# Performance work log

Hardware: AMD Instinct MI355X
Metric: run time of the kernel (lower is better)

Reference implementation:

```python
import jax, jax.numpy as jnp
import numpy as np

B, T, S = 8, 8192, 128
VD, LD, E, H = 256, 768, 256, 8
HD = E // H
SCALE = HD ** -0.5
NEG = -9e15


def setup_inputs() -> dict:
    key = jax.random.key(0)
    ks = jax.random.split(key, 16)
    def xavier(k, shape):
        fan_in, fan_out = shape[1], shape[0]
        lim = np.sqrt(6.0 / (fan_in + fan_out))
        return jax.random.uniform(k, shape, jnp.float32, -lim, lim)
    return {
        "v": jax.random.normal(ks[0], (B, T, VD), jnp.float32),
        "l": jax.random.normal(ks[1], (B, S, LD), jnp.float32),
        "v_pos": jax.random.normal(ks[2], (B, T, VD), jnp.float32),
        "attention_mask_l": jnp.ones((B, S), jnp.int32),
        "attention_mask_v": jnp.ones((B, T), jnp.int32),
        "Wv": xavier(ks[3], (E, VD)),  "bv": jnp.zeros((E,), jnp.float32),
        "Wl": xavier(ks[4], (E, LD)),  "bl": jnp.zeros((E,), jnp.float32),
        "Wvv": xavier(ks[5], (E, VD)), "bvv": jnp.zeros((E,), jnp.float32),
        "Wvl": xavier(ks[6], (E, LD)), "bvl": jnp.zeros((E,), jnp.float32),
        "Wov": xavier(ks[7], (VD, E)), "bov": jnp.zeros((VD,), jnp.float32),
        "Wol": xavier(ks[8], (LD, E)), "bol": jnp.zeros((LD,), jnp.float32),
    }


def _heads(x):  # [B, N, E] -> [B, H, N, HD]
    Bn, N, _ = x.shape
    return x.reshape(Bn, N, H, HD).transpose(0, 2, 1, 3)


def reference(v, l, v_pos, attention_mask_l, attention_mask_v,
              Wv, bv, Wl, bl, Wvv, bvv, Wvl, bvl, Wov, bov, Wol, bol):
    # projections
    q = _heads(((v + v_pos) @ Wv.T + bv) * SCALE)   # [B,H,T,HD]
    k = _heads(l @ Wl.T + bl)                        # [B,H,S,HD]
    val_v = _heads(v @ Wvv.T + bvv)                  # [B,H,T,HD]
    val_l = _heads(l @ Wvl.T + bvl)                  # [B,H,S,HD]

    # shared score matrix
    attn = jnp.einsum("bhtd,bhsd->bhts", q, k)       # [B,H,T,S]

    # language -> vision direction (softmax over vision tokens T)
    attn_T = attn.transpose(0, 1, 3, 2)              # [B,H,S,T]
    attn_l = attn_T - jnp.max(attn_T, axis=-1, keepdims=True)
    mv = attention_mask_v.astype(jnp.float32)
    add_v = jnp.where(mv == 0, NEG, mv)[:, None, None, :]  # [B,1,1,T]
    attn_l = jax.nn.softmax(attn_l + add_v, axis=-1)

    # vision -> language direction (softmax over language tokens S)
    ml = attention_mask_l.astype(jnp.float32)
    add_l = jnp.where(ml == 0, NEG, ml)[:, None, None, :]  # [B,1,1,S]
    attn_v = jax.nn.softmax(attn + add_l, axis=-1)

    # dropout p=0.1 is identity in eval mode
    out_v = jnp.einsum("bhts,bhsd->bhtd", attn_v, val_l)  # [B,H,T,HD]
    out_l = jnp.einsum("bhst,bhtd->bhsd", attn_l, val_v)  # [B,H,S,HD]

    out_v = out_v.transpose(0, 2, 1, 3).reshape(B, T, E) @ Wov.T + bov
    out_l = out_l.transpose(0, 2, 1, 3).reshape(B, S, E) @ Wol.T + bol
    return out_v, out_l
```

## Files before the change

kernel.cpp:

```cpp
#include <hip/hip_runtime.h>

#define B_ 8
#define T_ 8192
#define S_ 128
#define VD_ 256
#define LD_ 768
#define E_ 256
#define H_ 8
#define HD_ 32
#define TC_ 8
#define SCALE_ 0.17677669529663687f
#define NEG_ -9.0e15f
#define FIXM_ 40.0f

typedef __bf16 bf16x8 __attribute__((ext_vector_type(8)));
typedef float f32x4 __attribute__((ext_vector_type(4)));
typedef unsigned int uint4v __attribute__((ext_vector_type(4)));

__device__ inline float bf2f(unsigned short u) {
    return __uint_as_float(((unsigned int)u) << 16);
}
__device__ inline unsigned short f2bf(float f) {
    unsigned int u = __float_as_uint(f);
    u = u + 0x7FFFu + ((u >> 16) & 1u);
    return (unsigned short)(u >> 16);
}
__device__ inline unsigned int pkbf(float lo, float hi) {
    unsigned short a = __builtin_bit_cast(unsigned short, (__bf16)lo);
    unsigned short b = __builtin_bit_cast(unsigned short, (__bf16)hi);
    return (unsigned int)a | ((unsigned int)b << 16);
}
__device__ inline bf16x8 lds8(const unsigned short* p) {
    uint4v v = *reinterpret_cast<const uint4v*>(p);
    return __builtin_bit_cast(bf16x8, v);
}

template<typename T>
__device__ inline uint4v load8_as_bf16(const T* p);

template<> __device__ inline uint4v load8_as_bf16<unsigned short>(const unsigned short* p) {
    return *reinterpret_cast<const uint4v*>(p);
}
template<> __device__ inline uint4v load8_as_bf16<float>(const float* p) {
    f32x4 f0 = reinterpret_cast<const f32x4*>(p)[0];
    f32x4 f1 = reinterpret_cast<const f32x4*>(p)[1];
    uint4v r;
    #pragma unroll
    for (int jj = 0; jj < 2; ++jj) {
        r[jj]     = (unsigned int)f2bf(f0[jj*2]) | ((unsigned int)f2bf(f0[jj*2+1]) << 16);
        r[jj + 2] = (unsigned int)f2bf(f1[jj*2]) | ((unsigned int)f2bf(f1[jj*2+1]) << 16);
    }
    return r;
}
__device__ inline uint4v load8_add_as_bf16(const float* p, const float* p2) {
    f32x4 a0 = reinterpret_cast<const f32x4*>(p)[0];
    f32x4 a1 = reinterpret_cast<const f32x4*>(p)[1];
    f32x4 b0 = reinterpret_cast<const f32x4*>(p2)[0];
    f32x4 b1 = reinterpret_cast<const f32x4*>(p2)[1];
    a0 += b0; a1 += b1;
    uint4v r;
    #pragma unroll
    for (int jj = 0; jj < 2; ++jj) {
        r[jj]     = (unsigned int)f2bf(a0[jj*2]) | ((unsigned int)f2bf(a0[jj*2+1]) << 16);
        r[jj + 2] = (unsigned int)f2bf(a1[jj*2]) | ((unsigned int)f2bf(a1[jj*2+1]) << 16);
    }
    return r;
}

template<typename TA, typename TW, typename TOUT, bool HAS_A2, bool SCALED>
__global__ __launch_bounds__(256) void gemm_bt(
    const TA* __restrict__ A, const TA* __restrict__ A2,
    const TW* __restrict__ W, const float* __restrict__ bias,
    TOUT* __restrict__ C, int M, int N, int K, float scale)
{
    __shared__ __align__(16) unsigned short As[64][72];
    __shared__ __align__(16) unsigned short Ws[64][72];
    const int tid  = threadIdx.x;
    const int lane = tid & 63;
    const int w    = tid >> 6;
    const int wm   = w >> 1, wn = w & 1;
    const int m0   = blockIdx.x * 64, n0 = blockIdx.y * 64;
    const int row  = tid >> 2, c0 = tid & 3;
    const int qd   = lane >> 4, lr = lane & 15;
    const f32x4 zero = {0.f, 0.f, 0.f, 0.f};
    f32x4 acc[2][2] = {{zero, zero}, {zero, zero}};

    for (int k0 = 0; k0 < K; k0 += 64) {
        #pragma unroll
        for (int cc = 0; cc < 2; ++cc) {
            int c = c0 + cc * 4;
            const TA* pa = A + (size_t)(m0 + row) * K + k0 + c * 8;
            uint4v va;
            if constexpr (HAS_A2) {
                const TA* pa2 = A2 + (size_t)(m0 + row) * K + k0 + c * 8;
                va = load8_add_as_bf16(pa, pa2);
            } else {
                va = load8_as_bf16<TA>(pa);
            }
            *reinterpret_cast<uint4v*>(&As[row][c * 8]) = va;
            const TW* pw = W + (size_t)(n0 + row) * K + k0 + c * 8;
            *reinterpret_cast<uint4v*>(&Ws[row][c * 8]) = load8_as_bf16<TW>(pw);
        }
        __syncthreads();
        #pragma unroll
        for (int ks = 0; ks < 2; ++ks) {
            bf16x8 af[2], bfr[2];
            #pragma unroll
            for (int i = 0; i < 2; ++i)
                af[i] = lds8(&As[wm * 32 + i * 16 + lr][ks * 32 + qd * 8]);
            #pragma unroll
            for (int i = 0; i < 2; ++i)
                bfr[i] = lds8(&Ws[wn * 32 + i * 16 + lr][ks * 32 + qd * 8]);
            #pragma unroll
            for (int i = 0; i < 2; ++i)
                #pragma unroll
                for (int j = 0; j < 2; ++j)
                    acc[i][j] = __builtin_amdgcn_mfma_f32_16x16x32_bf16(
                        af[i], bfr[j], acc[i][j], 0, 0, 0);
        }
        __syncthreads();
    }
    #pragma unroll
    for (int j = 0; j < 2; ++j) {
        int col = n0 + wn * 32 + j * 16 + lr;
        float bval = bias[col];
        #pragma unroll
        for (int i = 0; i < 2; ++i) {
            int r0 = m0 + wm * 32 + i * 16 + qd * 4;
            #pragma unroll
            for (int r = 0; r < 4; ++r) {
                float v = acc[i][j][r] + bval;
                if (SCALED) v *= scale;
                if constexpr (sizeof(TOUT) == 2)
                    C[(size_t)(r0 + r) * N + col] = (TOUT)f2bf(v);
                else
                    C[(size_t)(r0 + r) * N + col] = (TOUT)v;
            }
        }
    }
}

template<typename TA, typename TOUT, bool HAS_A2, bool SCALED>
__global__ __launch_bounds__(1024) void gemm_ws(
    const TA* __restrict__ A, const float* __restrict__ A2,
    const float* __restrict__ Wf, const float* __restrict__ bias,
    TOUT* __restrict__ C, float scale)
{
    __shared__ __align__(16) unsigned short Ws[256 * 256];
    const int tid  = threadIdx.x;
    const int lane = tid & 63;
    const int w    = tid >> 6;
    const int quad = lane >> 4, lr = lane & 15;

    {
        const int row = tid >> 2;
        const int g0  = tid & 3;
        #pragma unroll
        for (int i = 0; i < 8; ++i) {
            const int g  = g0 + i * 4;
            const int gs = g ^ (row & 7);
            uint4v val = load8_as_bf16<float>(Wf + (size_t)row * 256 + g * 8);
            *reinterpret_cast<uint4v*>(&Ws[row * 256 + gs * 8]) = val;
        }
    }

    const int r0   = blockIdx.x * 256 + w * 16;
    const int arow = r0 + lr;
    bf16x8 af[8];
    #pragma unroll
    for (int kq = 0; kq < 8; ++kq) {
        if constexpr (sizeof(TA) == 2) {
            af[kq] = lds8(reinterpret_cast<const unsigned short*>(A)
                          + (size_t)arow * 256 + quad * 8 + kq * 32);
        } else {
            const float* pa = reinterpret_cast<const float*>(A)
                              + (size_t)arow * 256 + quad * 8 + kq * 32;
            f32x4 a0 = reinterpret_cast<const f32x4*>(pa)[0];
            f32x4 a1 = reinterpret_cast<const f32x4*>(pa)[1];
            if constexpr (HAS_A2) {
                const float* pp = A2 + (size_t)arow * 256 + quad * 8 + kq * 32;
                a0 += reinterpret_cast<const f32x4*>(pp)[0];
                a1 += reinterpret_cast<const f32x4*>(pp)[1];
            }
            uint4v u;
            u[0] = pkbf(a0[0], a0[1]); u[1] = pkbf(a0[2], a0[3]);
            u[2] = pkbf(a1[0], a1[1]); u[3] = pkbf(a1[2], a1[3]);
            af[kq] = __builtin_bit_cast(bf16x8, u);
        }
    }
    __syncthreads();

    const f32x4 zero = {0.f, 0.f, 0.f, 0.f};
    const int swz = lr & 7;
    for (int j = 0; j < 16; ++j) {
        const unsigned short* wbase = &Ws[(j * 16 + lr) * 256];
        f32x4 acc = zero;
        #pragma unroll
        for (int kq = 0; kq < 8; ++kq) {
            const int gs = (kq * 4 + quad) ^ swz;
            bf16x8 bw = lds8(wbase + gs * 8);
            acc = __builtin_amdgcn_mfma_f32_16x16x32_bf16(af[kq], bw, acc, 0, 0, 0);
        }
        const int col = j * 16 + lr;
        const float bval = bias[col];
        #pragma unroll
        for (int r = 0; r < 4; ++r) {
            float v0 = acc[r] + bval;
            if constexpr (SCALED) v0 *= scale;
            if constexpr (sizeof(TOUT) == 2)
                C[(size_t)(r0 + quad * 4 + r) * 256 + col] = (TOUT)f2bf(v0);
            else
                C[(size_t)(r0 + quad * 4 + r) * 256 + col] = (TOUT)v0;
        }
    }
}

__global__ __launch_bounds__(256) void attn_v_kernel(
    const unsigned short* __restrict__ q, const unsigned short* __restrict__ k,
    const unsigned short* __restrict__ vall, const int* __restrict__ mask_l,
    unsigned short* __restrict__ hv)
{
    __shared__ __align__(16) unsigned short Pl[64][136];
    __shared__ __align__(16) unsigned short Vt[32][136];
    const int tid  = threadIdx.x;
    const int lane = tid & 63;
    const int w    = tid >> 6;
    const int bh   = blockIdx.y, b = bh >> 3, h = bh & 7;
    const int t0   = blockIdx.x * 64;
    const int quad = lane >> 4, lr = lane & 15;
    const f32x4 zero = {0.f, 0.f, 0.f, 0.f};

    {
        int s = tid >> 1, dh = (tid & 1) * 16;
        const unsigned short* p = vall + (size_t)(b * S_ + s) * E_ + h * HD_ + dh;
        #pragma unroll
        for (int part = 0; part < 2; ++part) {
            uint4v v = reinterpret_cast<const uint4v*>(p)[part];
            #pragma unroll
            for (int jj = 0; jj < 4; ++jj) {
                unsigned int u = v[jj];
                int d = dh + part * 8 + jj * 2;
                Vt[d][s]     = (unsigned short)(u & 0xffffu);
                Vt[d + 1][s] = (unsigned short)(u >> 16);
            }
        }
    }

    bf16x8 afq = lds8(q + (size_t)(b * T_ + t0 + w * 16 + lr) * E_ + h * HD_ + quad * 8);
    f32x4 sc[8];
    #pragma unroll
    for (int n = 0; n < 8; ++n) {
        bf16x8 bk = lds8(k + (size_t)(b * S_ + n * 16 + lr) * E_ + h * HD_ + quad * 8);
        sc[n] = __builtin_amdgcn_mfma_f32_16x16x32_bf16(afq, bk, zero, 0, 0, 0);
    }
    #pragma unroll
    for (int n = 0; n < 8; ++n) {
        int s = n * 16 + lr;
        int mv = mask_l[b * S_ + s];
        float ad = (mv == 0) ? NEG_ : (float)mv;
        #pragma unroll
        for (int r = 0; r < 4; ++r) sc[n][r] += ad;
    }
    #pragma unroll
    for (int r = 0; r < 4; ++r) {
        float sum = 0.f;
        #pragma unroll
        for (int n = 0; n < 8; ++n) { float e = __expf(sc[n][r] - FIXM_); sc[n][r] = e; sum += e; }
        for (int off = 1; off < 16; off <<= 1) sum += __shfl_xor(sum, off);
        float inv = 1.0f / sum;
        #pragma unroll
        for (int n = 0; n < 8; ++n) sc[n][r] *= inv;
    }
    #pragma unroll
    for (int n = 0; n < 8; ++n)
        #pragma unroll
        for (int r = 0; r < 4; ++r)
            Pl[w * 16 + quad * 4 + r][n * 16 + lr] = f2bf(sc[n][r]);
    __syncthreads();
    f32x4 av[2] = {zero, zero};
    #pragma unroll
    for (int ks = 0; ks < 4; ++ks) {
        bf16x8 ap = lds8(&Pl[w * 16 + lr][ks * 32 + quad * 8]);
        #pragma unroll
        for (int nn = 0; nn < 2; ++nn) {
            bf16x8 bv = lds8(&Vt[nn * 16 + lr][ks * 32 + quad * 8]);
            av[nn] = __builtin_amdgcn_mfma_f32_16x16x32_bf16(ap, bv, av[nn], 0, 0, 0);
        }
    }
    #pragma unroll
    for (int nn = 0; nn < 2; ++nn)
        #pragma unroll
        for (int r = 0; r < 4; ++r) {
            int t = t0 + w * 16 + quad * 4 + r;
            hv[(size_t)(b * T_ + t) * E_ + h * HD_ + nn * 16 + lr] = f2bf(av[nn][r]);
        }
}

__global__ __launch_bounds__(512) void attn_l_kernel(
    const unsigned short* __restrict__ q, const unsigned short* __restrict__ k,
    const unsigned short* __restrict__ valv, const int* __restrict__ mask_v,
    float* __restrict__ pM, float* __restrict__ pL, float* __restrict__ pA)
{
    __shared__ __align__(16) unsigned short Et[128][136];
    __shared__ __align__(16) unsigned short Vt[32][136];
    const int tid  = threadIdx.x;
    const int lane = tid & 63;
    const int w    = tid >> 6;
    const int bh   = blockIdx.y, b = bh >> 3, h = bh & 7;
    const int chunk = blockIdx.x;
    const int quad = lane >> 4, lr = lane & 15;
    const int sw0  = w * 16;
    const f32x4 zero = {0.f, 0.f, 0.f, 0.f};

    bf16x8 kf = lds8(k + (size_t)(b * S_ + sw0 + lr) * E_ + h * HD_ + quad * 8);

    float lrun[4] = {0.f, 0.f, 0.f, 0.f};
    f32x4 accl[2] = {zero, zero};

    const int titer = T_ / TC_ / 128;
    for (int it = 0; it < titer; ++it) {
        int t0 = chunk * (T_ / TC_) + it * 128;
        __syncthreads();
        {
            int t = tid >> 2, dq = tid & 3;
            const unsigned short* p = valv + (size_t)(b * T_ + t0 + t) * E_ + h * HD_ + dq * 8;
            uint4v v = *reinterpret_cast<const uint4v*>(p);
            #pragma unroll
            for (int jj = 0; jj < 4; ++jj) {
                unsigned int u = v[jj];
                Vt[dq * 8 + jj * 2][t]     = (unsigned short)(u & 0xffffu);
                Vt[dq * 8 + jj * 2 + 1][t] = (unsigned short)(u >> 16);
            }
        }
        f32x4 sc[8];
        #pragma unroll
        for (int n = 0; n < 8; ++n) {
            bf16x8 qf = lds8(q + (size_t)(b * T_ + t0 + n * 16 + lr) * E_ + h * HD_ + quad * 8);
            sc[n] = __builtin_amdgcn_mfma_f32_16x16x32_bf16(kf, qf, zero, 0, 0, 0);
        }
        #pragma unroll
        for (int n = 0; n < 8; ++n) {
            int t = t0 + n * 16 + lr;
            int mv = mask_v[b * T_ + t];
            float ad = (mv == 0) ? NEG_ : (float)mv;
            #pragma unroll
            for (int r = 0; r < 4; ++r) sc[n][r] += ad;
        }
        #pragma unroll
        for (int r = 0; r < 4; ++r) {
            float sum = 0.f;
            #pragma unroll
            for (int n = 0; n < 8; ++n) {
                float e = __expf(sc[n][r] - FIXM_); sc[n][r] = e; sum += e;
            }
            for (int off = 1; off < 16; off <<= 1) sum += __shfl_xor(sum, off);
            lrun[r] += sum;
        }
        #pragma unroll
        for (int n = 0; n < 8; ++n)
            #pragma unroll
            for (int r = 0; r < 4; ++r)
                Et[sw0 + quad * 4 + r][n * 16 + lr] = f2bf(sc[n][r]);
        __syncthreads();
        #pragma unroll
        for (int ks = 0; ks < 4; ++ks) {
            bf16x8 ae = lds8(&Et[sw0 + lr][ks * 32 + quad * 8]);
            #pragma unroll
            for (int dn = 0; dn < 2; ++dn) {
                bf16x8 bv = lds8(&Vt[dn * 16 + lr][ks * 32 + quad * 8]);
                accl[dn] = __builtin_amdgcn_mfma_f32_16x16x32_bf16(ae, bv, accl[dn], 0, 0, 0);
            }
        }
    }
    int pc = bh * TC_ + chunk;
    #pragma unroll
    for (int r = 0; r < 4; ++r) {
        int s = sw0 + quad * 4 + r;
        if (lr == 0) {
            pM[(size_t)pc * 128 + s] = FIXM_;
            pL[(size_t)pc * 128 + s] = lrun[r];
        }
        #pragma unroll
        for (int dn = 0; dn < 2; ++dn)
            pA[((size_t)pc * 128 + s) * 32 + dn * 16 + lr] = accl[dn][r];
    }
}

__global__ __launch_bounds__(128) void combine_kernel(
    const float* __restrict__ pM, const float* __restrict__ pL,
    const float* __restrict__ pA, unsigned short* __restrict__ hl)
{
    int bh = blockIdx.x, b = bh >> 3, h = bh & 7;
    int s = threadIdx.x;
    float mc[TC_], wcf[TC_];
    float M = -3.0e38f;
    for (int c = 0; c < TC_; ++c) {
        mc[c] = pM[(size_t)(bh * TC_ + c) * 128 + s];
        M = fmaxf(M, mc[c]);
    }
    float L = 0.f;
    for (int c = 0; c < TC_; ++c) {
        wcf[c] = __expf(mc[c] - M);
        L += pL[(size_t)(bh * TC_ + c) * 128 + s] * wcf[c];
    }
    float inv = 1.0f / L;
    for (int d = 0; d < 32; ++d) {
        float o = 0.f;
        for (int c = 0; c < TC_; ++c)
            o += pA[((size_t)(bh * TC_ + c) * 128 + s) * 32 + d] * wcf[c];
        hl[(size_t)(b * S_ + s) * E_ + h * HD_ + d] = f2bf(o * inv);
    }
}

extern "C" void kernel_launch(void* const* d_in, const int* in_sizes, int n_in,
                              void* d_out, int out_size, void* d_ws, size_t ws_size,
                              hipStream_t stream)
{
    const float* v    = (const float*)d_in[0];
    const float* l    = (const float*)d_in[1];
    const float* vpos = (const float*)d_in[2];
    const int* mask_l = (const int*)d_in[3];
    const int* mask_v = (const int*)d_in[4];
    const float* Wv   = (const float*)d_in[5];
    const float* bv   = (const float*)d_in[6];
    const float* Wl   = (const float*)d_in[7];
    const float* bl   = (const float*)d_in[8];
    const float* Wvv  = (const float*)d_in[9];
    const float* bvv  = (const float*)d_in[10];
    const float* Wvl  = (const float*)d_in[11];
    const float* bvl  = (const float*)d_in[12];
    const float* Wov  = (const float*)d_in[13];
    const float* bov  = (const float*)d_in[14];
    const float* Wol  = (const float*)d_in[15];
    const float* bol  = (const float*)d_in[16];

    char* ws = (char*)d_ws;
    unsigned short* qbuf = (unsigned short*)(ws + 0);
    unsigned short* vbuf = (unsigned short*)(ws + 33554432);
    unsigned short* kbuf = (unsigned short*)(ws + 67108864);
    unsigned short* vall = (unsigned short*)(ws + 67633152);
    unsigned short* hl   = (unsigned short*)(ws + 68157440);
    float* pM            = (float*)(ws + 68681728);
    float* pL            = (float*)(ws + 68943872);
    float* pA            = (float*)(ws + 69206016);

    float* out_v = (float*)d_out;
    float* out_l = out_v + (size_t)B_ * T_ * VD_;

    gemm_ws<float, unsigned short, true, true>
        <<<dim3(B_*T_/256), 1024, 0, stream>>>(v, vpos, Wv, bv, qbuf, SCALE_);
    gemm_ws<float, unsigned short, false, false>
        <<<dim3(B_*T_/256), 1024, 0, stream>>>(v, nullptr, Wvv, bvv, vbuf, 1.f);

    gemm_bt<float, float, unsigned short, false, false>
        <<<dim3(B_*S_/64, E_/64), 256, 0, stream>>>(l, nullptr, Wl, bl, kbuf, B_*S_, E_, LD_, 1.f);
    gemm_bt<float, float, unsigned short, false, false>
        <<<dim3(B_*S_/64, E_/64), 256, 0, stream>>>(l, nullptr, Wvl, bvl, vall, B_*S_, E_, LD_, 1.f);

    attn_l_kernel<<<dim3(TC_, B_*H_), 512, 0, stream>>>(qbuf, kbuf, vbuf, mask_v, pM, pL, pA);
    combine_kernel<<<dim3(B_*H_), 128, 0, stream>>>(pM, pL, pA, hl);
    attn_v_kernel<<<dim3(T_/64, B_*H_), 256, 0, stream>>>(qbuf, kbuf, vall, mask_l, vbuf);

    gemm_ws<unsigned short, float, false, false>
        <<<dim3(B_*T_/256), 1024, 0, stream>>>(vbuf, nullptr, Wov, bov, out_v, 1.f);
    gemm_bt<unsigned short, float, float, false, false>
        <<<dim3(B_*S_/64, LD_/64), 256, 0, stream>>>(hl, nullptr, Wol, bol, out_l, B_*S_, LD_, E_, 1.f);
}
```

Measured before the change: 425.5 us.

## Interchange gemm_ws loops to k-outer with register-prefetched A fragments

Reorders the weight-stationary GEMM so the k loop is outermost, with 16 accumulators kept live across the output columns. Only one A fragment is held at a time, and the next one is prefetched from global memory during the MFMA work. The first A load is issued before the weight tile is staged into LDS, so global latency overlaps the LDS fill. This raises accumulator register use (64 floats) but lowers A fragment registers, which at 1024 threads per block may change spilling or occupancy.

```diff
diff --git a/kernel.cpp b/kernel.cpp
--- a/kernel.cpp
+++ b/kernel.cpp
@@ -151,6 +151,25 @@
     const int lane = tid & 63;
     const int w    = tid >> 6;
     const int quad = lane >> 4, lr = lane & 15;
+    const int r0   = blockIdx.x * 256 + w * 16;
+    const int arow = r0 + lr;
+
+    f32x4 pva0, pva1, pvb0, pvb1;
+    bf16x8 afp;
+    if constexpr (sizeof(TA) == 2) {
+        afp = lds8(reinterpret_cast<const unsigned short*>(A)
+                   + (size_t)arow * 256 + quad * 8);
+    } else {
+        const float* pa = reinterpret_cast<const float*>(A)
+                          + (size_t)arow * 256 + quad * 8;
+        pva0 = reinterpret_cast<const f32x4*>(pa)[0];
+        pva1 = reinterpret_cast<const f32x4*>(pa)[1];
+        if constexpr (HAS_A2) {
+            const float* pp = A2 + (size_t)arow * 256 + quad * 8;
+            pvb0 = reinterpret_cast<const f32x4*>(pp)[0];
+            pvb1 = reinterpret_cast<const f32x4*>(pp)[1];
+        }
+    }
 
     {
         const int row = tid >> 2;
@@ -163,49 +182,58 @@
             *reinterpret_cast<uint4v*>(&Ws[row * 256 + gs * 8]) = val;
         }
     }
-
-    const int r0   = blockIdx.x * 256 + w * 16;
-    const int arow = r0 + lr;
-    bf16x8 af[8];
+    __syncthreads();
+
+    const f32x4 zero = {0.f, 0.f, 0.f, 0.f};
+    f32x4 acc[16];
+    #pragma unroll
+    for (int j = 0; j < 16; ++j) acc[j] = zero;
+    const int swz = lr & 7;
+
     #pragma unroll
     for (int kq = 0; kq < 8; ++kq) {
+        bf16x8 af;
         if constexpr (sizeof(TA) == 2) {
-            af[kq] = lds8(reinterpret_cast<const unsigned short*>(A)
-                          + (size_t)arow * 256 + quad * 8 + kq * 32);
+            af = afp;
         } else {
-            const float* pa = reinterpret_cast<const float*>(A)
-                              + (size_t)arow * 256 + quad * 8 + kq * 32;
-            f32x4 a0 = reinterpret_cast<const f32x4*>(pa)[0];
-            f32x4 a1 = reinterpret_cast<const f32x4*>(pa)[1];
-            if constexpr (HAS_A2) {
-                const float* pp = A2 + (size_t)arow * 256 + quad * 8 + kq * 32;
-                a0 += reinterpret_cast<const f32x4*>(pp)[0];
-                a1 += reinterpret_cast<const f32x4*>(pp)[1];
-            }
+            f32x4 a0 = pva0, a1 = pva1;
+            if constexpr (HAS_A2) { a0 += pvb0; a1 += pvb1; }
             uint4v u;
             u[0] = pkbf(a0[0], a0[1]); u[1] = pkbf(a0[2], a0[3]);
             u[2] = pkbf(a1[0], a1[1]); u[3] = pkbf(a1[2], a1[3]);
-            af[kq] = __builtin_bit_cast(bf16x8, u);
-        }
-    }
-    __syncthreads();
-
-    const f32x4 zero = {0.f, 0.f, 0.f, 0.f};
-    const int swz = lr & 7;
+            af = __builtin_bit_cast(bf16x8, u);
+        }
+        if (kq < 7) {
+            if constexpr (sizeof(TA) == 2) {
+                afp = lds8(reinterpret_cast<const unsigned short*>(A)
+                           + (size_t)arow * 256 + quad * 8 + (kq + 1) * 32);
+            } else {
+                const float* pa = reinterpret_cast<const float*>(A)
+                                  + (size_t)arow * 256 + quad * 8 + (kq + 1) * 32;
+                pva0 = reinterpret_cast<const f32x4*>(pa)[0];
+                pva1 = reinterpret_cast<const f32x4*>(pa)[1];
+                if constexpr (HAS_A2) {
+                    const float* pp = A2 + (size_t)arow * 256 + quad * 8 + (kq + 1) * 32;
+                    pvb0 = reinterpret_cast<const f32x4*>(pp)[0];
+                    pvb1 = reinterpret_cast<const f32x4*>(pp)[1];
+                }
+            }
+        }
+        const int gs = ((kq * 4 + quad) ^ swz) * 8;
+        #pragma unroll
+        for (int j = 0; j < 16; ++j) {
+            bf16x8 bw = lds8(&Ws[(j * 16 + lr) * 256 + gs]);
+            acc[j] = __builtin_amdgcn_mfma_f32_16x16x32_bf16(af, bw, acc[j], 0, 0, 0);
+        }
+    }
+
+    #pragma unroll
     for (int j = 0; j < 16; ++j) {
-        const unsigned short* wbase = &Ws[(j * 16 + lr) * 256];
-        f32x4 acc = zero;
-        #pragma unroll
-        for (int kq = 0; kq < 8; ++kq) {
-            const int gs = (kq * 4 + quad) ^ swz;
-            bf16x8 bw = lds8(wbase + gs * 8);
-            acc = __builtin_amdgcn_mfma_f32_16x16x32_bf16(af[kq], bw, acc, 0, 0, 0);
-        }
         const int col = j * 16 + lr;
         const float bval = bias[col];
         #pragma unroll
         for (int r = 0; r < 4; ++r) {
-            float v0 = acc[r] + bval;
+            float v0 = acc[j][r] + bval;
             if constexpr (SCALED) v0 *= scale;
             if constexpr (sizeof(TOUT) == 2)
                 C[(size_t)(r0 + quad * 4 + r) * 256 + col] = (TOUT)f2bf(v0);
```

Result: no change. 427.9 us (+0.5%).
